# Performance work log

Hardware: AMD Instinct MI355X
Metric: run time of the kernel (lower is better)

## Reference

```python
import jax, jax.numpy as jnp
import numpy as np

EPS_ATTN = 1e-6
EPS_LN = 1e-5  # torch nn.LayerNorm default eps
NHEAD = 8
L, D, DFF, S, B = 4, 512, 1024, 4096, 8


def _layernorm(x, g, b):
    m = jnp.mean(x, axis=-1, keepdims=True)
    v = jnp.mean((x - m) ** 2, axis=-1, keepdims=True)
    return (x - m) * jax.lax.rsqrt(v + EPS_LN) * g + b


def _layer(src, Wq, bq, Wk, bk, Wv, bv, Wo, bo, g1, be1, W1, bf1, W2, bf2, g2, be2):
    # src: (S, B, D)
    s, b, d = src.shape
    dk = d // NHEAD
    Q = (src @ Wq + bq).reshape(s, b, NHEAD, dk)
    K = (src @ Wk + bk).reshape(s, b, NHEAD, dk)
    V = (src @ Wv + bv).reshape(s, b, NHEAD, dk)
    # ELU+1 feature-map linear attention, vectorized over heads
    phiQ = jax.nn.elu(Q) + 1.0
    phiK = jax.nn.elu(K) + 1.0
    context = jnp.einsum('sbhd,sbhe->bhde', phiK, V)          # (B,H,dk,dk)
    out = jnp.einsum('sbhd,bhde->sbhe', phiQ, context)        # (S,B,H,dk)
    denom = jnp.einsum('sbhd,bhd->sbh', phiQ, phiK.sum(0))    # (S,B,H)
    out = out / (denom[..., None] + EPS_ATTN)
    attn = out.reshape(s, b, d)  # concat heads (same order as torch cat)
    out = attn @ Wo + bo
    out = _layernorm(src + out, g1, be1)
    ffn = jax.nn.relu(out @ W1 + bf1) @ W2 + bf2
    return _layernorm(out + ffn, g2, be2)


def setup_inputs() -> dict:
    key = jax.random.key(0)
    ks = jax.random.split(key, 8)
    sc = 0.02
    inp = {
        'src': jax.random.normal(ks[0], (S, B, D), jnp.float32),
        'Wq': jax.random.normal(ks[1], (L, D, D), jnp.float32) * sc,
        'bq': jnp.zeros((L, D), jnp.float32),
        'Wk': jax.random.normal(ks[2], (L, D, D), jnp.float32) * sc,
        'bk': jnp.zeros((L, D), jnp.float32),
        'Wv': jax.random.normal(ks[3], (L, D, D), jnp.float32) * sc,
        'bv': jnp.zeros((L, D), jnp.float32),
        'Wo': jax.random.normal(ks[4], (L, D, D), jnp.float32) * sc,
        'bo': jnp.zeros((L, D), jnp.float32),
        'ln1_g': jnp.ones((L, D), jnp.float32),
        'ln1_b': jnp.zeros((L, D), jnp.float32),
        'W1': jax.random.normal(ks[5], (L, D, DFF), jnp.float32) * sc,
        'b1': jnp.zeros((L, DFF), jnp.float32),
        'W2': jax.random.normal(ks[6], (L, DFF, D), jnp.float32) * sc,
        'b2': jnp.zeros((L, D), jnp.float32),
        'ln2_g': jnp.ones((L, D), jnp.float32),
        'ln2_b': jnp.zeros((L, D), jnp.float32),
    }
    return inp


def reference(src, Wq, bq, Wk, bk, Wv, bv, Wo, bo, ln1_g, ln1_b, W1, b1, W2, b2, ln2_g, ln2_b):
    x = src
    for i in range(Wq.shape[0]):  # small fixed layer count
        x = _layer(x, Wq[i], bq[i], Wk[i], bk[i], Wv[i], bv[i], Wo[i], bo[i],
                   ln1_g[i], ln1_b[i], W1[i], b1[i], W2[i], b2[i], ln2_g[i], ln2_b[i])
    return x
```

## Files before the change

kernel.cpp:

```cpp
#include <hip/hip_runtime.h>
#include <hip/hip_bf16.h>
#include <cstdint>

typedef __attribute__((ext_vector_type(8))) short short8;
typedef __attribute__((ext_vector_type(4))) float f32x4;
typedef __attribute__((ext_vector_type(4))) unsigned short ushort4v;

#define DEV static __device__ __forceinline__

DEV float bf2f(unsigned short u) {
    union { unsigned int i; float f; } v; v.i = ((unsigned int)u) << 16; return v.f;
}
DEV unsigned short f2bf(float f) {
    union { float f; unsigned int i; } v; v.f = f;
    unsigned int x = v.i;
    unsigned int r = x + 0x7fffu + ((x >> 16) & 1u);
    return (unsigned short)(r >> 16);
}

template<int EPI>
__global__ __launch_bounds__(256) void gemm_kernel(
    const unsigned short* __restrict__ A, int lda,
    const unsigned short* __restrict__ Bt,
    const float* __restrict__ bias,
    unsigned short* __restrict__ outp, int ldc,
    int nshift, int K)
{
    __shared__ unsigned short lds[128 * 136];
    const int t  = threadIdx.x;
    const int w  = t >> 6, l = t & 63;
    const int wr = w >> 1, wc = w & 1;
    const int lr = l & 15, lg = l >> 4;
    const int bid = blockIdx.x;
    const int j8  = bid & 7, s = bid >> 3;
    const int bx  = j8 * 32 + (s >> nshift);
    const int by  = s & ((1 << nshift) - 1);
    const long tM = (long)bx * 128;
    const long tN = (long)by * 128;

    f32x4 acc[4][4];
#pragma unroll
    for (int i = 0; i < 4; i++)
#pragma unroll
        for (int j = 0; j < 4; j++) acc[i][j] = f32x4{0.f, 0.f, 0.f, 0.f};

    const unsigned short* Ab = A  + tM * lda;
    const unsigned short* Bb = Bt + tN * K;

    for (int kt = 0; kt < K; kt += 64) {
#pragma unroll
        for (int j = 0; j < 4; j++) {
            int c = (w * 4 + j) * 64 + l;
            int row = c >> 3, sc = (c & 7) ^ (row & 7);
            __builtin_amdgcn_global_load_lds(
                (const __attribute__((address_space(1))) void*)(Ab + (long)row * lda + kt + sc * 8),
                (__attribute__((address_space(3))) void*)(lds + (w * 4 + j) * 512),
                16, 0, 0);
        }
#pragma unroll
        for (int j = 0; j < 4; j++) {
            int c = (w * 4 + j) * 64 + l;
            int row = c >> 3, sc = (c & 7) ^ (row & 7);
            __builtin_amdgcn_global_load_lds(
                (const __attribute__((address_space(1))) void*)(Bb + (long)row * K + kt + sc * 8),
                (__attribute__((address_space(3))) void*)(lds + 8192 + (w * 4 + j) * 512),
                16, 0, 0);
        }
        __syncthreads();
#pragma unroll
        for (int kk = 0; kk < 2; kk++) {
            short8 af[4], bfv[4];
#pragma unroll
            for (int mi = 0; mi < 4; mi++) {
                int r  = wr * 64 + mi * 16 + lr;
                int kc = kk * 4 + lg;
                af[mi] = *(const short8*)&lds[r * 64 + ((kc ^ (r & 7)) << 3)];
            }
#pragma unroll
            for (int ni = 0; ni < 4; ni++) {
                int n  = wc * 64 + ni * 16 + lr;
                int kc = kk * 4 + lg;
                bfv[ni] = *(const short8*)&lds[8192 + n * 64 + ((kc ^ (n & 7)) << 3)];
            }
#pragma unroll
            for (int mi = 0; mi < 4; mi++)
#pragma unroll
                for (int ni = 0; ni < 4; ni++)
                    acc[mi][ni] = __builtin_amdgcn_mfma_f32_16x16x32_bf16(
                        af[mi], bfv[ni], acc[mi][ni], 0, 0, 0);
        }
        __syncthreads();
    }

    float bv[4];
#pragma unroll
    for (int ni = 0; ni < 4; ni++) bv[ni] = bias[tN + wc * 64 + ni * 16 + lr];
    const bool doElu = (EPI == 0) && (tN < 512);

#pragma unroll
    for (int mi = 0; mi < 4; mi++)
#pragma unroll
        for (int ni = 0; ni < 4; ni++)
#pragma unroll
            for (int j = 0; j < 4; j++) {
                float v = acc[mi][ni][j] + bv[ni];
                if (EPI == 0) { if (doElu) v = (v > 0.f) ? (v + 1.f) : expf(v); }
                if (EPI == 2) v = fmaxf(v, 0.f);
                int r = wr * 64 + mi * 16 + lg * 4 + j;
                int c = wc * 64 + ni * 16 + lr;
                lds[r * 136 + c] = f2bf(v);
            }
    __syncthreads();
#pragma unroll
    for (int i = 0; i < 8; i++) {
        int q = i * 256 + t;
        int r = q >> 4, cc = q & 15;
        short8 v8 = *(const short8*)&lds[r * 136 + cc * 8];
        *(short8*)&outp[(tM + r) * ldc + tN + cc * 8] = v8;
    }
}

__global__ __launch_bounds__(512) void gemm_ln_kernel(
    const unsigned short* __restrict__ A, int lda,
    const unsigned short* __restrict__ Bt,
    const float* __restrict__ bias,
    const float* __restrict__ res,
    const float* __restrict__ g,
    const float* __restrict__ be,
    float* __restrict__ of,
    unsigned short* __restrict__ ob,
    int K)
{
    __shared__ unsigned short sA[2][128 * 32];
    __shared__ unsigned short sB[2][512 * 32];
    float* redb  = (float*)&sA[0][0];
    float* statb = redb + 1024;
    const int t = threadIdx.x, w = t >> 6, l = t & 63, lr = l & 15, lg = l >> 4;
    const int wr = w >> 2, wc = w & 3;
    const long tM = (long)blockIdx.x * 128;

    f32x4 acc[4][8];
#pragma unroll
    for (int i = 0; i < 4; i++)
#pragma unroll
        for (int j = 0; j < 8; j++) acc[i][j] = f32x4{0.f, 0.f, 0.f, 0.f};

    const unsigned short* Ab = A + tM * lda;

    auto STAGE = [&](int buf, int kt) {
        {
            int c = t, row = c >> 2, sc = (c & 3) ^ ((row >> 1) & 3);
            __builtin_amdgcn_global_load_lds(
                (const __attribute__((address_space(1))) void*)(Ab + (long)row * lda + kt + sc * 8),
                (__attribute__((address_space(3))) void*)(&sA[buf][t * 8]),
                16, 0, 0);
        }
#pragma unroll
        for (int j = 0; j < 4; j++) {
            int c = j * 512 + t, row = c >> 2, sc = (c & 3) ^ ((row >> 1) & 3);
            __builtin_amdgcn_global_load_lds(
                (const __attribute__((address_space(1))) void*)(Bt + (long)row * K + kt + sc * 8),
                (__attribute__((address_space(3))) void*)(&sB[buf][c * 8]),
                16, 0, 0);
        }
    };

    auto COMPUTE = [&](int buf) {
        short8 av[4], bw[8];
#pragma unroll
        for (int mi = 0; mi < 4; mi++) {
            int r = wr * 64 + mi * 16 + lr;
            av[mi] = *(const short8*)&sA[buf][r * 32 + ((lg ^ ((r >> 1) & 3)) << 3)];
        }
#pragma unroll
        for (int ni = 0; ni < 8; ni++) {
            int n = wc * 128 + ni * 16 + lr;
            bw[ni] = *(const short8*)&sB[buf][n * 32 + ((lg ^ ((n >> 1) & 3)) << 3)];
        }
#pragma unroll
        for (int mi = 0; mi < 4; mi++)
#pragma unroll
            for (int ni = 0; ni < 8; ni++)
                acc[mi][ni] = __builtin_amdgcn_mfma_f32_16x16x32_bf16(
                    av[mi], bw[ni], acc[mi][ni], 0, 0, 0);
    };

    STAGE(0, 0);
    __syncthreads();
    int cur = 0;
    for (int kt = 32; kt < K; kt += 32) {
        STAGE(cur ^ 1, kt);
        COMPUTE(cur);
        __syncthreads();
        cur ^= 1;
    }
    COMPUTE(cur);

    float gv[8], bev[8], bb[8];
#pragma unroll
    for (int ni = 0; ni < 8; ni++) {
        int col = wc * 128 + ni * 16 + lr;
        gv[ni] = g[col]; bev[ni] = be[col]; bb[ni] = bias[col];
    }
#pragma unroll
    for (int mi = 0; mi < 4; mi++)
#pragma unroll
        for (int jj = 0; jj < 4; jj++) {
            long row = tM + wr * 64 + mi * 16 + lg * 4 + jj;
#pragma unroll
            for (int ni = 0; ni < 8; ni++) {
                int col = wc * 128 + ni * 16 + lr;
                acc[mi][ni][jj] += bb[ni] + res[row * 512 + col];
            }
        }
    float s2[4][4], ss2[4][4];
#pragma unroll
    for (int mi = 0; mi < 4; mi++)
#pragma unroll
        for (int jj = 0; jj < 4; jj++) {
            float s = 0.f, ss = 0.f;
#pragma unroll
            for (int ni = 0; ni < 8; ni++) {
                float v = acc[mi][ni][jj];
                s += v; ss += v * v;
            }
#pragma unroll
            for (int off = 1; off < 16; off <<= 1) {
                s  += __shfl_xor(s, off);
                ss += __shfl_xor(ss, off);
            }
            s2[mi][jj] = s; ss2[mi][jj] = ss;
        }
    __syncthreads();
    if (lr == 0) {
#pragma unroll
        for (int mi = 0; mi < 4; mi++)
#pragma unroll
            for (int jj = 0; jj < 4; jj++) {
                int rb = wr * 64 + mi * 16 + lg * 4 + jj;
                redb[0 * 512 + wc * 128 + rb] = s2[mi][jj];
                redb[1 * 512 + wc * 128 + rb] = ss2[mi][jj];
            }
    }
    __syncthreads();
    if (t < 128) {
        float S  = redb[t] + redb[128 + t] + redb[256 + t] + redb[384 + t];
        float SS = redb[512 + t] + redb[640 + t] + redb[768 + t] + redb[896 + t];
        float mean = S * (1.0f / 512.0f);
        float var  = SS * (1.0f / 512.0f) - mean * mean;
        statb[t] = mean;
        statb[128 + t] = rsqrtf(fmaxf(var, 0.f) + 1e-5f);
    }
    __syncthreads();
#pragma unroll
    for (int mi = 0; mi < 4; mi++)
#pragma unroll
        for (int jj = 0; jj < 4; jj++) {
            int rb = wr * 64 + mi * 16 + lg * 4 + jj;
            long row = tM + rb;
            float mean = statb[rb], rstd = statb[128 + rb];
#pragma unroll
            for (int ni = 0; ni < 8; ni++) {
                int col = wc * 128 + ni * 16 + lr;
                float y = (acc[mi][ni][jj] - mean) * rstd * gv[ni] + bev[ni];
                of[row * 512 + col] = y;
                ob[row * 512 + col] = f2bf(y);
            }
        }
}

__global__ __launch_bounds__(256) void ctx_partial_kernel(
    const unsigned short* __restrict__ kv, float* __restrict__ part,
    float* __restrict__ part2)
{
    const int p = blockIdx.x, ch = blockIdx.y;
    const int b = p >> 3, h = p & 7;
    __shared__ float kb[64 * 68];
    __shared__ float vbuf[64 * 68];
    const int t = threadIdx.x;
    const int dq = t >> 4, eq = t & 15;
    f32x4 acc[4];
    f32x4 ks = {0.f, 0.f, 0.f, 0.f};
#pragma unroll
    for (int i = 0; i < 4; i++) acc[i] = f32x4{0.f, 0.f, 0.f, 0.f};

    for (int sub = 0; sub < 8; sub++) {
        int sbase = ch * 512 + sub * 64;
#pragma unroll
        for (int i = 0; i < 2; i++) {
            int idx = i * 256 + t;
            int row = idx >> 3, c8 = idx & 7;
            long ga = ((long)(sbase + row) * 8 + b) * 1024 + h * 64 + c8 * 8;
            short8 kvv = *(const short8*)&kv[ga];
            short8 vv  = *(const short8*)&kv[ga + 512];
#pragma unroll
            for (int j = 0; j < 8; j++) {
                kb[row * 68 + c8 * 8 + j]   = bf2f((unsigned short)kvv[j]);
                vbuf[row * 68 + c8 * 8 + j] = bf2f((unsigned short)vv[j]);
            }
        }
        __syncthreads();
        for (int s = 0; s < 64; s++) {
            f32x4 k4 = *(const f32x4*)&kb[s * 68 + dq * 4];
            f32x4 v4 = *(const f32x4*)&vbuf[s * 68 + eq * 4];
#pragma unroll
            for (int i = 0; i < 4; i++) acc[i] += k4[i] * v4;
            ks += k4;
        }
        __syncthreads();
    }
    float* o = part + (long)(p * 8 + ch) * 4096;
#pragma unroll
    for (int i = 0; i < 4; i++)
        *(f32x4*)&o[(dq * 4 + i) * 64 + eq * 4] = acc[i];
    if (eq == 0)
        *(f32x4*)&part2[(p * 8 + ch) * 64 + dq * 4] = ks;
}

__global__ __launch_bounds__(256) void ctx_reduce_kernel(
    const float* __restrict__ part, const float* __restrict__ part2,
    unsigned short* __restrict__ ctxA)
{
    int o = (blockIdx.x * 256 + threadIdx.x) * 4;
    int p = o >> 12, d = (o >> 6) & 63, e0 = o & 63;
    f32x4 s = {0.f, 0.f, 0.f, 0.f};
    for (int ch = 0; ch < 8; ch++)
        s += *(const f32x4*)&part[(long)(p * 8 + ch) * 4096 + d * 64 + e0];
#pragma unroll
    for (int j = 0; j < 4; j++) ctxA[p * 5120 + (e0 + j) * 64 + d] = f2bf(s[j]);
    if (e0 == 0) {
        float ksv = 0.f;
#pragma unroll
        for (int ch = 0; ch < 8; ch++) ksv += part2[(p * 8 + ch) * 64 + d];
        ctxA[p * 5120 + 4096 + d] = f2bf(ksv);
#pragma unroll
        for (int j = 1; j < 16; j++) ctxA[p * 5120 + 4096 + j * 64 + d] = 0;
    }
}

__global__ __launch_bounds__(256) void attn_out_kernel(
    unsigned short* __restrict__ kv,
    const unsigned short* __restrict__ ctxA)
{
    const int p = blockIdx.x;
    const int b = p >> 3, h = p & 7;
    const int t = threadIdx.x, w = t >> 6, l = t & 63, lr = l & 15, lg = l >> 4;
    const int s0 = blockIdx.y * 256 + w * 64;
    f32x4 acc[4][5];
#pragma unroll
    for (int i = 0; i < 4; i++)
#pragma unroll
        for (int j = 0; j < 5; j++) acc[i][j] = f32x4{0.f, 0.f, 0.f, 0.f};
    const unsigned short* cb = ctxA + p * 5120;
#pragma unroll
    for (int kk = 0; kk < 2; kk++) {
        short8 af[4], bfv[5];
#pragma unroll
        for (int mi = 0; mi < 4; mi++) {
            int s = s0 + mi * 16 + lr;
            af[mi] = *(const short8*)&kv[((long)s * 8 + b) * 1024 + 512 + h * 64 + kk * 32 + lg * 8];
        }
#pragma unroll
        for (int ni = 0; ni < 5; ni++)
            bfv[ni] = *(const short8*)&cb[(ni * 16 + lr) * 64 + kk * 32 + lg * 8];
#pragma unroll
        for (int mi = 0; mi < 4; mi++)
#pragma unroll
            for (int ni = 0; ni < 5; ni++)
                acc[mi][ni] = __builtin_amdgcn_mfma_f32_16x16x32_bf16(
                    af[mi], bfv[ni], acc[mi][ni], 0, 0, 0);
    }
#pragma unroll
    for (int mi = 0; mi < 4; mi++) {
#pragma unroll
        for (int j = 0; j < 4; j++) {
            float den = __shfl(acc[mi][4][j], (l & 48));
            float rc  = 1.0f / (den + 1e-6f);
            int s = s0 + mi * 16 + lg * 4 + j;
            long base = ((long)s * 8 + b) * 1024 + h * 64;
#pragma unroll
            for (int ni = 0; ni < 4; ni++)
                kv[base + ni * 16 + lr] = f2bf(acc[mi][ni][j] * rc);
        }
    }
}

__global__ __launch_bounds__(256) void cvtbf_kernel(
    const float* __restrict__ x, unsigned short* __restrict__ y)
{
    long i = ((long)blockIdx.x * 256 + threadIdx.x) * 8;
    f32x4 a = *(const f32x4*)&x[i];
    f32x4 c = *(const f32x4*)&x[i + 4];
    short8 pk;
#pragma unroll
    for (int j = 0; j < 4; j++) { pk[j] = (short)f2bf(a[j]); pk[4 + j] = (short)f2bf(c[j]); }
    *(short8*)&y[i] = pk;
}

__global__ __launch_bounds__(256) void bcat_kernel(
    const float* __restrict__ bk, const float* __restrict__ bv, float* __restrict__ dst)
{
    int lyr = blockIdx.x;
    int j = blockIdx.y * 256 + threadIdx.x;
    dst[lyr * 1024 + j] = (j < 512) ? bk[lyr * 512 + j] : bv[lyr * 512 + j - 512];
}

__global__ __launch_bounds__(256) void wconv_kernel(
    const float* __restrict__ W, unsigned short* __restrict__ Wt, int K, int N,
    long lstrW, long lstrT)
{
    __shared__ float tile[64 * 65];
    const long lz = blockIdx.z;
    const float* Wl = W + lz * lstrW;
    unsigned short* Wtl = Wt + lz * lstrT;
    const int k0 = blockIdx.x * 64, n0 = blockIdx.y * 64;
    const int t = threadIdx.x;
#pragma unroll
    for (int i = 0; i < 4; i++) {
        int q = i * 256 + t;
        int r = q >> 4, c4 = q & 15;
        f32x4 v = *(const f32x4*)&Wl[(long)(k0 + r) * N + n0 + c4 * 4];
#pragma unroll
        for (int j = 0; j < 4; j++) tile[r * 65 + c4 * 4 + j] = v[j];
    }
    __syncthreads();
#pragma unroll
    for (int i = 0; i < 4; i++) {
        int q = i * 256 + t;
        int nr = q >> 4, kc = q & 15;
        ushort4v pk;
#pragma unroll
        for (int j = 0; j < 4; j++) pk[j] = f2bf(tile[(kc * 4 + j) * 65 + nr]);
        *(ushort4v*)&Wtl[(long)(n0 + nr) * K + k0 + kc * 4] = pk;
    }
}

extern "C" void kernel_launch(void* const* d_in, const int* in_sizes, int n_in,
                              void* d_out, int out_size, void* d_ws, size_t ws_size,
                              hipStream_t stream)
{
    const float* src  = (const float*)d_in[0];
    const float* Wq   = (const float*)d_in[1];
    const float* bq   = (const float*)d_in[2];
    const float* Wk   = (const float*)d_in[3];
    const float* bk   = (const float*)d_in[4];
    const float* Wv   = (const float*)d_in[5];
    const float* bv   = (const float*)d_in[6];
    const float* Wo   = (const float*)d_in[7];
    const float* bo   = (const float*)d_in[8];
    const float* l1g  = (const float*)d_in[9];
    const float* l1b  = (const float*)d_in[10];
    const float* W1   = (const float*)d_in[11];
    const float* b1   = (const float*)d_in[12];
    const float* W2   = (const float*)d_in[13];
    const float* b2   = (const float*)d_in[14];
    const float* l2g  = (const float*)d_in[15];
    const float* l2b  = (const float*)d_in[16];

    char* ws = (char*)d_ws;
    constexpr size_t SZ_WKV = (size_t)4 * 1024 * 512 * 2;
    constexpr size_t SZ_WQ  = (size_t)4 * 512 * 512 * 2;
    constexpr size_t SZ_WO  = SZ_WQ;
    constexpr size_t SZ_W1  = (size_t)4 * 512 * 1024 * 2;
    constexpr size_t SZ_W2  = SZ_W1;
    constexpr size_t SZ_BKV = (size_t)4 * 1024 * 4;
    constexpr size_t SZ_R1  = (size_t)32768 * 512 * 2;
    constexpr size_t SZ_KV  = (size_t)32768 * 1024 * 2;
    constexpr size_t OFF_WKV = 0;
    constexpr size_t OFF_WQ  = OFF_WKV + SZ_WKV;
    constexpr size_t OFF_WO  = OFF_WQ + SZ_WQ;
    constexpr size_t OFF_W1  = OFF_WO + SZ_WO;
    constexpr size_t OFF_W2  = OFF_W1 + SZ_W1;
    constexpr size_t OFF_BKV = OFF_W2 + SZ_W2;
    constexpr size_t OFF_R1  = OFF_BKV + SZ_BKV;
    constexpr size_t OFF_KV  = OFF_R1 + SZ_R1;
    constexpr size_t OFF_KSP = OFF_KV + SZ_KV;
    constexpr size_t OFF_CTP = OFF_KSP + (size_t)16 * 4096 * 4;
    constexpr size_t OFF_CTA = OFF_CTP + (size_t)64 * 8 * 4096 * 4;

    unsigned short* WKVT = (unsigned short*)(ws + OFF_WKV);
    unsigned short* WQT  = (unsigned short*)(ws + OFF_WQ);
    unsigned short* WOT  = (unsigned short*)(ws + OFF_WO);
    unsigned short* W1T  = (unsigned short*)(ws + OFF_W1);
    unsigned short* W2T  = (unsigned short*)(ws + OFF_W2);
    float*          BKV  = (float*)(ws + OFF_BKV);
    unsigned short* R1   = (unsigned short*)(ws + OFF_R1);
    unsigned short* KV   = (unsigned short*)(ws + OFF_KV);
    float*          KSP  = (float*)(ws + OFF_KSP);
    float*          CTP  = (float*)(ws + OFF_CTP);
    unsigned short* CTA  = (unsigned short*)(ws + OFF_CTA);
    float*          F1   = (float*)d_out;

    dim3 blk(256);
    wconv_kernel<<<dim3(8, 8, 4),  blk, 0, stream>>>(Wk, WKVT,            512, 512, 512*512, 1024*512);
    wconv_kernel<<<dim3(8, 8, 4),  blk, 0, stream>>>(Wv, WKVT + 512*512,  512, 512, 512*512, 1024*512);
    wconv_kernel<<<dim3(8, 8, 4),  blk, 0, stream>>>(Wq, WQT,             512, 512, 512*512, 512*512);
    wconv_kernel<<<dim3(8, 8, 4),  blk, 0, stream>>>(Wo, WOT,             512, 512, 512*512, 512*512);
    wconv_kernel<<<dim3(8, 16, 4), blk, 0, stream>>>(W1, W1T,             512, 1024, 512*1024, 512*1024);
    wconv_kernel<<<dim3(16, 8, 4), blk, 0, stream>>>(W2, W2T,             1024, 512, 1024*512, 1024*512);
    bcat_kernel<<<dim3(4, 4), blk, 0, stream>>>(bk, bv, BKV);
    cvtbf_kernel<<<8192, blk, 0, stream>>>(src, R1);

    for (int lyr = 0; lyr < 4; lyr++) {
        const unsigned short* wkvt = WKVT + (size_t)lyr * 1024 * 512;
        const unsigned short* wqt  = WQT  + (size_t)lyr * 512 * 512;
        const unsigned short* wot  = WOT  + (size_t)lyr * 512 * 512;
        const unsigned short* w1t  = W1T  + (size_t)lyr * 512 * 1024;
        const unsigned short* w2t  = W2T  + (size_t)lyr * 1024 * 512;

        gemm_kernel<0><<<2048, blk, 0, stream>>>(R1, 512, wkvt, BKV + lyr * 1024, KV, 1024, 3, 512);

        ctx_partial_kernel<<<dim3(64, 8), blk, 0, stream>>>(KV, CTP, KSP);
        ctx_reduce_kernel<<<256, blk, 0, stream>>>(CTP, KSP, CTA);

        gemm_kernel<0><<<1024, blk, 0, stream>>>(R1, 512, wqt, bq + lyr * 512, KV + 512, 1024, 2, 512);
        attn_out_kernel<<<dim3(64, 16), blk, 0, stream>>>(KV, CTA);

        const float* resp = (lyr == 0) ? src : F1;
        gemm_ln_kernel<<<256, dim3(512), 0, stream>>>(KV, 1024, wot, bo + lyr * 512, resp,
                                                      l1g + lyr * 512, l1b + lyr * 512,
                                                      F1, R1, 512);
        gemm_kernel<2><<<2048, blk, 0, stream>>>(R1, 512, w1t, b1 + lyr * 1024, KV, 1024, 3, 512);
        gemm_ln_kernel<<<256, dim3(512), 0, stream>>>(KV, 1024, w2t, b2 + lyr * 512, F1,
                                                      l2g + lyr * 512, l2b + lyr * 512,
                                                      F1, R1, 1024);
    }
}
```

Before: 1.314 ms.

## Double-buffer GEMM K-loop and carry the LN1 residual in bf16

The generic GEMM kernel moves from a single-buffered BK=64 loop with two barriers per step to a double-buffered BK=32 loop. The next tile's global-to-LDS copy is issued before the current tile's MFMAs, so load latency can overlap compute, and a new swizzle matches the narrower tile. The layer-norm GEMM becomes templated so the first LN skips writing its fp32 output. The second LN then reads its residual from the bf16 copy, which saves global traffic but adds bf16 rounding on the residual path. The global_load_lds LDS destinations are also changed to per-wave base addresses.

```diff
diff --git a/kernel.cpp b/kernel.cpp
--- a/kernel.cpp
+++ b/kernel.cpp
@@ -47,50 +47,60 @@
     const unsigned short* Ab = A  + tM * lda;
     const unsigned short* Bb = Bt + tN * K;
 
-    for (int kt = 0; kt < K; kt += 64) {
-#pragma unroll
-        for (int j = 0; j < 4; j++) {
-            int c = (w * 4 + j) * 64 + l;
-            int row = c >> 3, sc = (c & 7) ^ (row & 7);
+    auto STAGE = [&](int buf, int kt) {
+        const int base = buf * 8192;
+#pragma unroll
+        for (int j = 0; j < 2; j++) {
+            int c = j * 256 + w * 64 + l;
+            int row = c >> 2, sc = (c & 3) ^ ((row >> 1) & 3);
             __builtin_amdgcn_global_load_lds(
                 (const __attribute__((address_space(1))) void*)(Ab + (long)row * lda + kt + sc * 8),
-                (__attribute__((address_space(3))) void*)(lds + (w * 4 + j) * 512),
+                (__attribute__((address_space(3))) void*)(lds + base + (j * 256 + w * 64) * 8),
                 16, 0, 0);
         }
 #pragma unroll
-        for (int j = 0; j < 4; j++) {
-            int c = (w * 4 + j) * 64 + l;
-            int row = c >> 3, sc = (c & 7) ^ (row & 7);
+        for (int j = 0; j < 2; j++) {
+            int c = j * 256 + w * 64 + l;
+            int row = c >> 2, sc = (c & 3) ^ ((row >> 1) & 3);
             __builtin_amdgcn_global_load_lds(
                 (const __attribute__((address_space(1))) void*)(Bb + (long)row * K + kt + sc * 8),
-                (__attribute__((address_space(3))) void*)(lds + 8192 + (w * 4 + j) * 512),
+                (__attribute__((address_space(3))) void*)(lds + base + 4096 + (j * 256 + w * 64) * 8),
                 16, 0, 0);
         }
+    };
+
+    auto COMPUTE = [&](int buf) {
+        const int base = buf * 8192;
+        short8 af[4], bfv[4];
+#pragma unroll
+        for (int mi = 0; mi < 4; mi++) {
+            int r = wr * 64 + mi * 16 + lr;
+            af[mi] = *(const short8*)&lds[base + r * 32 + ((lg ^ ((r >> 1) & 3)) << 3)];
+        }
+#pragma unroll
+        for (int ni = 0; ni < 4; ni++) {
+            int n = wc * 64 + ni * 16 + lr;
+            bfv[ni] = *(const short8*)&lds[base + 4096 + n * 32 + ((lg ^ ((n >> 1) & 3)) << 3)];
+        }
+#pragma unroll
+        for (int mi = 0; mi < 4; mi++)
+#pragma unroll
+            for (int ni = 0; ni < 4; ni++)
+                acc[mi][ni] = __builtin_amdgcn_mfma_f32_16x16x32_bf16(
+                    af[mi], bfv[ni], acc[mi][ni], 0, 0, 0);
+    };
+
+    STAGE(0, 0);
+    __syncthreads();
+    int cur = 0;
+    for (int kt = 32; kt < K; kt += 32) {
+        STAGE(cur ^ 1, kt);
+        COMPUTE(cur);
         __syncthreads();
-#pragma unroll
-        for (int kk = 0; kk < 2; kk++) {
-            short8 af[4], bfv[4];
-#pragma unroll
-            for (int mi = 0; mi < 4; mi++) {
-                int r  = wr * 64 + mi * 16 + lr;
-                int kc = kk * 4 + lg;
-                af[mi] = *(const short8*)&lds[r * 64 + ((kc ^ (r & 7)) << 3)];
-            }
-#pragma unroll
-            for (int ni = 0; ni < 4; ni++) {
-                int n  = wc * 64 + ni * 16 + lr;
-                int kc = kk * 4 + lg;
-                bfv[ni] = *(const short8*)&lds[8192 + n * 64 + ((kc ^ (n & 7)) << 3)];
-            }
-#pragma unroll
-            for (int mi = 0; mi < 4; mi++)
-#pragma unroll
-                for (int ni = 0; ni < 4; ni++)
-                    acc[mi][ni] = __builtin_amdgcn_mfma_f32_16x16x32_bf16(
-                        af[mi], bfv[ni], acc[mi][ni], 0, 0, 0);
-        }
-        __syncthreads();
-    }
+        cur ^= 1;
+    }
+    COMPUTE(cur);
+    __syncthreads();
 
     float bv[4];
 #pragma unroll
@@ -120,11 +130,12 @@
     }
 }
 
+template<int RESBF, int WRITEOF>
 __global__ __launch_bounds__(512) void gemm_ln_kernel(
     const unsigned short* __restrict__ A, int lda,
     const unsigned short* __restrict__ Bt,
     const float* __restrict__ bias,
-    const float* __restrict__ res,
+    const void* __restrict__ resp,
     const float* __restrict__ g,
     const float* __restrict__ be,
     float* __restrict__ of,
@@ -152,7 +163,7 @@
             int c = t, row = c >> 2, sc = (c & 3) ^ ((row >> 1) & 3);
             __builtin_amdgcn_global_load_lds(
                 (const __attribute__((address_space(1))) void*)(Ab + (long)row * lda + kt + sc * 8),
-                (__attribute__((address_space(3))) void*)(&sA[buf][t * 8]),
+                (__attribute__((address_space(3))) void*)(&sA[buf][(w * 64) * 8]),
                 16, 0, 0);
         }
 #pragma unroll
@@ -160,7 +171,7 @@
             int c = j * 512 + t, row = c >> 2, sc = (c & 3) ^ ((row >> 1) & 3);
             __builtin_amdgcn_global_load_lds(
                 (const __attribute__((address_space(1))) void*)(Bt + (long)row * K + kt + sc * 8),
-                (__attribute__((address_space(3))) void*)(&sB[buf][c * 8]),
+                (__attribute__((address_space(3))) void*)(&sB[buf][(j * 512 + w * 64) * 8]),
                 16, 0, 0);
         }
     };
@@ -196,6 +207,8 @@
     }
     COMPUTE(cur);
 
+    const float* resf = (const float*)resp;
+    const unsigned short* resb = (const unsigned short*)resp;
     float gv[8], bev[8], bb[8];
 #pragma unroll
     for (int ni = 0; ni < 8; ni++) {
@@ -210,7 +223,8 @@
 #pragma unroll
             for (int ni = 0; ni < 8; ni++) {
                 int col = wc * 128 + ni * 16 + lr;
-                acc[mi][ni][jj] += bb[ni] + res[row * 512 + col];
+                float rv = RESBF ? bf2f(resb[row * 512 + col]) : resf[row * 512 + col];
+                acc[mi][ni][jj] += bb[ni] + rv;
             }
         }
     float s2[4][4], ss2[4][4];
@@ -263,7 +277,7 @@
             for (int ni = 0; ni < 8; ni++) {
                 int col = wc * 128 + ni * 16 + lr;
                 float y = (acc[mi][ni][jj] - mean) * rstd * gv[ni] + bev[ni];
-                of[row * 512 + col] = y;
+                if (WRITEOF) of[row * 512 + col] = y;
                 ob[row * 512 + col] = f2bf(y);
             }
         }
@@ -516,13 +530,13 @@
         gemm_kernel<0><<<1024, blk, 0, stream>>>(R1, 512, wqt, bq + lyr * 512, KV + 512, 1024, 2, 512);
         attn_out_kernel<<<dim3(64, 16), blk, 0, stream>>>(KV, CTA);
 
-        const float* resp = (lyr == 0) ? src : F1;
-        gemm_ln_kernel<<<256, dim3(512), 0, stream>>>(KV, 1024, wot, bo + lyr * 512, resp,
-                                                      l1g + lyr * 512, l1b + lyr * 512,
-                                                      F1, R1, 512);
+        const void* resp = (lyr == 0) ? (const void*)src : (const void*)F1;
+        gemm_ln_kernel<0, 0><<<256, dim3(512), 0, stream>>>(KV, 1024, wot, bo + lyr * 512, resp,
+                                                            l1g + lyr * 512, l1b + lyr * 512,
+                                                            F1, R1, 512);
         gemm_kernel<2><<<2048, blk, 0, stream>>>(R1, 512, w1t, b1 + lyr * 1024, KV, 1024, 3, 512);
-        gemm_ln_kernel<<<256, dim3(512), 0, stream>>>(KV, 1024, w2t, b2 + lyr * 512, F1,
-                                                      l2g + lyr * 512, l2b + lyr * 512,
-                                                      F1, R1, 1024);
-    }
-}
+        gemm_ln_kernel<1, 1><<<256, dim3(512), 0, stream>>>(KV, 1024, w2t, b2 + lyr * 512, R1,
+                                                            l2g + lyr * 512, l2b + lyr * 512,
+                                                            F1, R1, 1024);
+    }
+}
```

Measured after the change: 1.299 ms. No clear change (-1.1%).
